# Kernel optimization log

Measured on AMD Instinct MI355X. Metric: run time of the kernel, lower is better.

The kernel has to match this reference:

```python
import jax, jax.numpy as jnp
import numpy as np

VOCAB, EMB, HID, LAT = 32000, 512, 1024, 64
B, S = 64, 512

def setup_inputs() -> dict:
    key = jax.random.key(0)
    ks = jax.random.split(key, 10)
    s_e = 1.0 / np.sqrt(HID)
    s_l = 1.0 / np.sqrt(HID)
    return {
        'input_ids': jax.random.randint(ks[0], (B, S), 0, VOCAB),
        'emb_weight': jax.random.normal(ks[1], (VOCAB, EMB), jnp.float32),
        'w_ih': jax.random.uniform(ks[2], (3 * HID, EMB), jnp.float32, -s_e, s_e),
        'w_hh': jax.random.uniform(ks[3], (3 * HID, HID), jnp.float32, -s_e, s_e),
        'b_ih': jax.random.uniform(ks[4], (3 * HID,), jnp.float32, -s_e, s_e),
        'b_hh': jax.random.uniform(ks[5], (3 * HID,), jnp.float32, -s_e, s_e),
        'w_mean': jax.random.uniform(ks[6], (LAT, HID), jnp.float32, -s_l, s_l),
        'b_mean': jax.random.uniform(ks[7], (LAT,), jnp.float32, -s_l, s_l),
        'w_logv': jax.random.uniform(ks[8], (LAT, HID), jnp.float32, -s_l, s_l),
        'b_logv': jax.random.uniform(ks[9], (LAT,), jnp.float32, -s_l, s_l),
    }

def _gru_mean_hidden(ids, emb_weight, w_ih, w_hh, b_ih, b_hh):
    x = emb_weight[ids]                      # [B, S, E]
    # precompute input-side gate preactivations for all timesteps
    gx = jnp.einsum('bse,ge->bsg', x, w_ih) + b_ih   # [B, S, 3H]
    gx_t = jnp.swapaxes(gx, 0, 1)            # [S, B, 3H] for scan

    def step(h, gx_i):
        gh = h @ w_hh.T + b_hh               # [B, 3H]
        # torch GRU gate order: r, z, n
        r = jax.nn.sigmoid(gx_i[:, :HID] + gh[:, :HID])
        z = jax.nn.sigmoid(gx_i[:, HID:2 * HID] + gh[:, HID:2 * HID])
        n = jnp.tanh(gx_i[:, 2 * HID:] + r * gh[:, 2 * HID:])
        h_new = (1.0 - z) * n + z * h
        return h_new, h_new

    h0 = jnp.zeros((ids.shape[0], HID), gx.dtype)
    _, hs = jax.lax.scan(step, h0, gx_t)      # hs: [S, B, H]
    return jnp.mean(hs, axis=0)               # mean pooling over time -> [B, H]

def reference(input_ids, emb_weight, w_ih, w_hh, b_ih, b_hh, w_mean, b_mean, w_logv, b_logv):
    h = _gru_mean_hidden(input_ids, emb_weight, w_ih, w_hh, b_ih, b_hh)
    mean = h @ w_mean.T + b_mean
    logv = h @ w_logv.T + b_logv
    return (mean, logv)
```

## Files before the change

kernel.cpp:

```cpp
#include <hip/hip_runtime.h>
#include <hip/hip_bf16.h>
#include <stdint.h>
#include <stddef.h>

#define HID   1024
#define NB    64
#define SEQ   512
#define G3    3072
#define EMB   512
#define LAT   64

typedef __attribute__((ext_vector_type(4))) float f32x4;
typedef __attribute__((ext_vector_type(8))) short bfrag;
typedef unsigned long long ull;

__device__ __forceinline__ unsigned short f2bf(float x) {
  union { float f; unsigned u; } v; v.f = x;
  unsigned u = v.u + 0x7fffu + ((v.u >> 16) & 1u);
  return (unsigned short)(u >> 16);
}
__device__ __forceinline__ float bf2f(short s) {
  union { unsigned u; float f; } v; v.u = ((unsigned)(unsigned short)s) << 16;
  return v.f;
}
__device__ __forceinline__ float fsig(float x) {
  return 1.0f / (1.0f + __builtin_exp2f(-1.4426950408889634f * x));
}
__device__ __forceinline__ float ftanh(float x) {
  return 1.0f - 2.0f / (1.0f + __builtin_exp2f(2.8853900817779268f * x));
}
__device__ __forceinline__ void gload_lds16(const void* g, void* l) {
  __builtin_amdgcn_global_load_lds(
      (const __attribute__((address_space(1))) unsigned int*)g,
      (__attribute__((address_space(3))) unsigned int*)l, 16, 0, 0);
}

__global__ void cvt_wih_kernel(const float* __restrict__ in, short* __restrict__ out) {
  int i = (blockIdx.x * 256 + threadIdx.x) * 8;
  f32x4 a = *(const f32x4*)(in + i);
  f32x4 b = *(const f32x4*)(in + i + 4);
  bfrag o;
  o[0]=(short)f2bf(a[0]); o[1]=(short)f2bf(a[1]); o[2]=(short)f2bf(a[2]); o[3]=(short)f2bf(a[3]);
  o[4]=(short)f2bf(b[0]); o[5]=(short)f2bf(b[1]); o[6]=(short)f2bf(b[2]); o[7]=(short)f2bf(b[3]);
  *(bfrag*)(out + i) = o;
}

__global__ void __launch_bounds__(256) gemm_gx_kernel(
    const int* __restrict__ ids, const float* __restrict__ emb,
    const short* __restrict__ wih, short* __restrict__ gx)
{
  const int nt = blockIdx.x, mt = blockIdx.y;
  const int tid = threadIdx.x;
  const int lane = tid & 63, wave = tid >> 6;
  const int wr = wave >> 1, wc = wave & 1;

  __shared__ __align__(16) short A_lds[128 * 48];
  __shared__ __align__(16) short B_lds[128 * 32];
  __shared__ int ids_s[128];

  if (tid < 128) ids_s[tid] = ids[mt * 128 + tid];
  __syncthreads();

  f32x4 acc[4][4];
  #pragma unroll
  for (int i = 0; i < 4; ++i)
    #pragma unroll
    for (int j = 0; j < 4; ++j) acc[i][j] = (f32x4){0.f, 0.f, 0.f, 0.f};

  const int r_stage = tid >> 1;
  const int kh = (tid & 1) * 16;

  #pragma unroll 1
  for (int kc = 0; kc < 16; ++kc) {
    __syncthreads();
    {
      const float* src = emb + (size_t)ids_s[r_stage] * 512 + kc * 32 + kh;
      f32x4 v0 = *(const f32x4*)(src);
      f32x4 v1 = *(const f32x4*)(src + 4);
      f32x4 v2 = *(const f32x4*)(src + 8);
      f32x4 v3 = *(const f32x4*)(src + 12);
      bfrag p0, p1;
      p0[0]=(short)f2bf(v0[0]); p0[1]=(short)f2bf(v0[1]); p0[2]=(short)f2bf(v0[2]); p0[3]=(short)f2bf(v0[3]);
      p0[4]=(short)f2bf(v1[0]); p0[5]=(short)f2bf(v1[1]); p0[6]=(short)f2bf(v1[2]); p0[7]=(short)f2bf(v1[3]);
      p1[0]=(short)f2bf(v2[0]); p1[1]=(short)f2bf(v2[1]); p1[2]=(short)f2bf(v2[2]); p1[3]=(short)f2bf(v2[3]);
      p1[4]=(short)f2bf(v3[0]); p1[5]=(short)f2bf(v3[1]); p1[6]=(short)f2bf(v3[2]); p1[7]=(short)f2bf(v3[3]);
      *(bfrag*)&A_lds[r_stage * 48 + kh]     = p0;
      *(bfrag*)&A_lds[r_stage * 48 + kh + 8] = p1;
    }
    {
      #pragma unroll
      for (int ii = 0; ii < 2; ++ii) {
        int i = wave * 2 + ii;
        const short* src = wih + (size_t)(nt * 128 + i * 16 + (lane >> 2)) * 512
                               + kc * 32 + (lane & 3) * 8;
        gload_lds16((const void*)src, (void*)&B_lds[i * 512]);
      }
    }
    asm volatile("s_waitcnt vmcnt(0)" ::: "memory");
    __syncthreads();

    bfrag a[4], b[4];
    #pragma unroll
    for (int mi = 0; mi < 4; ++mi)
      a[mi] = *(const bfrag*)&A_lds[(wr * 64 + mi * 16 + (lane & 15)) * 48 + (lane >> 4) * 8];
    #pragma unroll
    for (int ni = 0; ni < 4; ++ni)
      b[ni] = *(const bfrag*)&B_lds[(wc * 64 + ni * 16 + (lane & 15)) * 32 + (lane >> 4) * 8];
    #pragma unroll
    for (int mi = 0; mi < 4; ++mi)
      #pragma unroll
      for (int ni = 0; ni < 4; ++ni)
        acc[mi][ni] = __builtin_amdgcn_mfma_f32_16x16x32_bf16(a[mi], b[ni], acc[mi][ni], 0, 0, 0);
  }

  #pragma unroll
  for (int mi = 0; mi < 4; ++mi)
    #pragma unroll
    for (int ni = 0; ni < 4; ++ni)
      #pragma unroll
      for (int r = 0; r < 4; ++r) {
        int m = mt * 128 + wr * 64 + mi * 16 + (lane >> 4) * 4 + r;
        int n = nt * 128 + wc * 64 + ni * 16 + (lane & 15);
        gx[(size_t)m * G3 + n] = (short)f2bf(acc[mi][ni][r]);
      }
}

__global__ void __launch_bounds__(256, 1) gru_scan_kernel(
    const short* __restrict__ gx, const float* __restrict__ whh,
    const float* __restrict__ bihp, const float* __restrict__ bhhp,
    ull* __restrict__ hbuf_q, unsigned int* __restrict__ flags,
    float* __restrict__ hsum)
{
  const int wg   = blockIdx.x;
  const int team = wg >> 6;
  const int cg   = wg & 63;
  const int tid  = threadIdx.x;
  const int lane = tid & 63, wave = tid >> 6;
  const int bl   = lane & 15;
  const int bsub = (lane >> 4) * 4;
  const int jcol = cg * 16 + bl;
  const int bteam = team * 16;

  __shared__ __align__(16) short h_lds[16 * 1024];
  __shared__ __align__(16) float part[3 * 3 * 256];
  __shared__ __align__(16) short hstg[256];

  bfrag wfrag[3][8];
  #pragma unroll
  for (int g = 0; g < 3; ++g) {
    const float* wrow = whh + (size_t)(g * 1024 + jcol) * 1024 + wave * 256 + (lane >> 4) * 8;
    #pragma unroll
    for (int ks = 0; ks < 8; ++ks) {
      const float* p = wrow + ks * 32;
      f32x4 lo = *(const f32x4*)p;
      f32x4 hi = *(const f32x4*)(p + 4);
      bfrag f;
      f[0]=(short)f2bf(lo[0]); f[1]=(short)f2bf(lo[1]); f[2]=(short)f2bf(lo[2]); f[3]=(short)f2bf(lo[3]);
      f[4]=(short)f2bf(hi[0]); f[5]=(short)f2bf(hi[1]); f[6]=(short)f2bf(hi[2]); f[7]=(short)f2bf(hi[3]);
      wfrag[g][ks] = f;
    }
  }
  float bih_r[3], bhh_r[3];
  #pragma unroll
  for (int g = 0; g < 3; ++g) {
    bih_r[g] = bihp[g * 1024 + jcol];
    bhh_r[g] = bhhp[g * 1024 + jcol];
  }

  float hprev[4] = {0.f, 0.f, 0.f, 0.f};
  float hacc[4]  = {0.f, 0.f, 0.f, 0.f};
  const int xorm = (bl & 7) << 4;
  const char* lbase = (const char*)h_lds + bl * 2048;
  unsigned int* fteam = flags + team * 1024;
  unsigned int* myflag = fteam + cg * 16;

  short gxr_[4][3];
  if (wave == 0) {
    #pragma unroll
    for (int r = 0; r < 4; ++r) {
      size_t base = ((size_t)(bteam + bsub + r) * SEQ + 0) * G3 + jcol;
      gxr_[r][0] = gx[base];
      gxr_[r][1] = gx[base + 1024];
      gxr_[r][2] = gx[base + 2048];
    }
  }

  #pragma unroll 1
  for (int s = 0; s < SEQ; ++s) {
    const ull* hsrc = hbuf_q + ((s & 1) ? 16384 : 0) + team * 4096;
    ull*       hdst = hbuf_q + (((s + 1) & 1) ? 16384 : 0) + team * 4096;

    {
      ull hv[16];
      #pragma unroll
      for (int j = 0; j < 16; ++j)
        hv[j] = __hip_atomic_load(hsrc + j * 256 + tid, __ATOMIC_RELAXED,
                                  __HIP_MEMORY_SCOPE_AGENT);
      #pragma unroll
      for (int j = 0; j < 16; ++j) {
        int q  = j * 256 + tid;
        int cgq = q >> 6, b = (q >> 2) & 15, cq = q & 3;
        *(ull*)((char*)h_lds + b * 2048 + ((cgq * 32 + cq * 8) ^ ((b & 7) << 4))) = hv[j];
      }
    }
    __syncthreads();

    f32x4 a0 = {0.f,0.f,0.f,0.f}, a1 = {0.f,0.f,0.f,0.f}, a2 = {0.f,0.f,0.f,0.f};
    #pragma unroll
    for (int ks = 0; ks < 8; ++ks) {
      int k2 = wave * 512 + ks * 64 + (lane >> 4) * 16;
      bfrag af = *(const bfrag*)(lbase + (k2 ^ xorm));
      a0 = __builtin_amdgcn_mfma_f32_16x16x32_bf16(af, wfrag[0][ks], a0, 0, 0, 0);
      a1 = __builtin_amdgcn_mfma_f32_16x16x32_bf16(af, wfrag[1][ks], a1, 0, 0, 0);
      a2 = __builtin_amdgcn_mfma_f32_16x16x32_bf16(af, wfrag[2][ks], a2, 0, 0, 0);
    }
    if (wave) {
      int w1 = wave - 1;
      *(f32x4*)&part[((0 * 3 + w1) * 64 + lane) * 4] = a0;
      *(f32x4*)&part[((1 * 3 + w1) * 64 + lane) * 4] = a1;
      *(f32x4*)&part[((2 * 3 + w1) * 64 + lane) * 4] = a2;
    }
    __syncthreads();

    if (wave == 0) {
      f32x4 s0 = a0, s1 = a1, s2 = a2;
      #pragma unroll
      for (int w1 = 0; w1 < 3; ++w1) {
        s0 += *(const f32x4*)&part[((0 * 3 + w1) * 64 + lane) * 4];
        s1 += *(const f32x4*)&part[((1 * 3 + w1) * 64 + lane) * 4];
        s2 += *(const f32x4*)&part[((2 * 3 + w1) * 64 + lane) * 4];
      }
      #pragma unroll
      for (int r = 0; r < 4; ++r) {
        float ghr = s0[r] + bhh_r[0];
        float ghz = s1[r] + bhh_r[1];
        float ghn = s2[r] + bhh_r[2];
        float rg = fsig(bf2f(gxr_[r][0]) + bih_r[0] + ghr);
        float zg = fsig(bf2f(gxr_[r][1]) + bih_r[1] + ghz);
        float ng = ftanh(bf2f(gxr_[r][2]) + bih_r[2] + rg * ghn);
        float hn = (1.f - zg) * ng + zg * hprev[r];
        hprev[r] = hn;
        hacc[r] += hn;
        hstg[(bsub + r) * 16 + bl] = (short)f2bf(hn);
      }
    }
    __syncthreads();

    if (wave == 1) {
      ull v = ((const ull*)hstg)[lane];
      __hip_atomic_store(hdst + cg * 64 + lane, v, __ATOMIC_RELAXED,
                         __HIP_MEMORY_SCOPE_AGENT);
      asm volatile("s_waitcnt vmcnt(0)" ::: "memory");
      if (lane == 0)
        __hip_atomic_store(myflag, (unsigned)(s + 1), __ATOMIC_RELAXED,
                           __HIP_MEMORY_SCOPE_AGENT);
    }
    if (wave == 0) {
      int sn = (s + 1 < SEQ) ? (s + 1) : s;
      #pragma unroll
      for (int r = 0; r < 4; ++r) {
        size_t base = ((size_t)(bteam + bsub + r) * SEQ + sn) * G3 + jcol;
        gxr_[r][0] = gx[base];
        gxr_[r][1] = gx[base + 1024];
        gxr_[r][2] = gx[base + 2048];
      }
      unsigned tgt = (unsigned)(s + 1);
      for (;;) {
        unsigned v = __hip_atomic_load(fteam + lane * 16, __ATOMIC_RELAXED,
                                       __HIP_MEMORY_SCOPE_AGENT);
        if (__all((int)(v >= tgt))) break;
      }
    }
    __syncthreads();
  }

  if (wave == 0) {
    #pragma unroll
    for (int r = 0; r < 4; ++r)
      hsum[(size_t)(bteam + bsub + r) * 1024 + jcol] = hacc[r] * (1.0f / 512.0f);
  }
}

__global__ void proj_kernel(const float* __restrict__ hbar,
                            const float* __restrict__ wm, const float* __restrict__ bm,
                            const float* __restrict__ wl, const float* __restrict__ bl,
                            float* __restrict__ out)
{
  int b = blockIdx.x, t = threadIdx.x;
  __shared__ float hrow[1024];
  for (int k = t; k < 1024; k += 128) hrow[k] = hbar[(size_t)b * 1024 + k];
  __syncthreads();
  int j = t & 63;
  const float* w = (t < 64) ? (wm + (size_t)j * 1024) : (wl + (size_t)j * 1024);
  float acc = (t < 64) ? bm[j] : bl[j];
  for (int k = 0; k < 1024; k += 4) {
    f32x4 wv = *(const f32x4*)(w + k);
    acc += hrow[k] * wv[0] + hrow[k+1] * wv[1] + hrow[k+2] * wv[2] + hrow[k+3] * wv[3];
  }
  out[(size_t)((t < 64) ? 0 : 4096) + b * 64 + j] = acc;
}

extern "C" void kernel_launch(void* const* d_in, const int* in_sizes, int n_in,
                              void* d_out, int out_size, void* d_ws, size_t ws_size,
                              hipStream_t stream) {
  const int*   ids   = (const int*)d_in[0];
  const float* emb   = (const float*)d_in[1];
  const float* w_ih  = (const float*)d_in[2];
  const float* w_hh  = (const float*)d_in[3];
  const float* b_ih  = (const float*)d_in[4];
  const float* b_hh  = (const float*)d_in[5];
  const float* w_mean= (const float*)d_in[6];
  const float* b_mean= (const float*)d_in[7];
  const float* w_logv= (const float*)d_in[8];
  const float* b_logv= (const float*)d_in[9];
  float* out = (float*)d_out;

  char* ws = (char*)d_ws;
  unsigned int* flags = (unsigned int*)(ws);
  ull* hbuf_q        = (ull*)(ws + 16384);
  float* hsum        = (float*)(ws + 16384 + 262144);
  short* wihb        = (short*)(ws + 16384 + 262144 + 262144);
  short* gxbuf       = (short*)(ws + 16384 + 262144 + 262144 + 3145728);

  hipMemsetAsync(ws, 0, 16384 + 262144, stream);

  cvt_wih_kernel<<<768, 256, 0, stream>>>(w_ih, wihb);
  gemm_gx_kernel<<<dim3(24, 256), 256, 0, stream>>>(ids, emb, wihb, gxbuf);
  gru_scan_kernel<<<256, 256, 0, stream>>>(gxbuf, w_hh, b_ih, b_hh, hbuf_q, flags, hsum);
  proj_kernel<<<64, 128, 0, stream>>>(hsum, w_mean, b_mean, w_logv, b_logv, out);
}
```

Before: 2.031 ms.

## Replace flag-based grid barrier with epoch-tagged hidden-state words

Each published bf16 hidden value is now packed with a 16-bit step epoch in its upper half, so consumers spin directly on the data words until the expected epoch appears. This removes the separate per-workgroup flag store, the vmcnt wait before it, the flag polling loop and two block-wide barriers per timestep. The cost is doubled hidden-state traffic, since each value now occupies 32 bits, plus per-word polling. The design relies on relaxed 64-bit atomics not tearing and on the epoch not wrapping within 512 steps.

```diff
diff --git a/kernel.cpp b/kernel.cpp
--- a/kernel.cpp
+++ b/kernel.cpp
@@ -128,8 +128,7 @@
 __global__ void __launch_bounds__(256, 1) gru_scan_kernel(
     const short* __restrict__ gx, const float* __restrict__ whh,
     const float* __restrict__ bihp, const float* __restrict__ bhhp,
-    ull* __restrict__ hbuf_q, unsigned int* __restrict__ flags,
-    float* __restrict__ hsum)
+    ull* __restrict__ hbuf_q, float* __restrict__ hsum)
 {
   const int wg   = blockIdx.x;
   const int team = wg >> 6;
@@ -143,7 +142,7 @@
 
   __shared__ __align__(16) short h_lds[16 * 1024];
   __shared__ __align__(16) float part[3 * 3 * 256];
-  __shared__ __align__(16) short hstg[256];
+  __shared__ __align__(16) unsigned hstg[256];
 
   bfrag wfrag[3][8];
   #pragma unroll
@@ -171,8 +170,6 @@
   float hacc[4]  = {0.f, 0.f, 0.f, 0.f};
   const int xorm = (bl & 7) << 4;
   const char* lbase = (const char*)h_lds + bl * 2048;
-  unsigned int* fteam = flags + team * 1024;
-  unsigned int* myflag = fteam + cg * 16;
 
   short gxr_[4][3];
   if (wave == 0) {
@@ -187,23 +184,34 @@
 
   #pragma unroll 1
   for (int s = 0; s < SEQ; ++s) {
-    const ull* hsrc = hbuf_q + ((s & 1) ? 16384 : 0) + team * 4096;
-    ull*       hdst = hbuf_q + (((s + 1) & 1) ? 16384 : 0) + team * 4096;
+    const ull* qsrc = hbuf_q + ((s & 1) ? 32768 : 0) + team * 8192;
+    ull*       qdst = hbuf_q + (((s + 1) & 1) ? 32768 : 0) + team * 8192;
 
     {
-      ull hv[16];
-      #pragma unroll
-      for (int j = 0; j < 16; ++j)
-        hv[j] = __hip_atomic_load(hsrc + j * 256 + tid, __ATOMIC_RELAXED,
-                                  __HIP_MEMORY_SCOPE_AGENT);
-      #pragma unroll
-      for (int j = 0; j < 16; ++j) {
-        int q  = j * 256 + tid;
-        int cgq = q >> 6, b = (q >> 2) & 15, cq = q & 3;
-        *(ull*)((char*)h_lds + b * 2048 + ((cgq * 32 + cq * 8) ^ ((b & 7) << 4))) = hv[j];
-      }
-    }
-    __syncthreads();
+      const ull want = (ull)(unsigned)s * 0x0001000000010000ull;
+      ull hv[32];
+      #pragma unroll
+      for (int b = 0; b < 16; ++b) {
+        hv[2*b]   = __hip_atomic_load(qsrc + b * 512 + wave * 128 + lane,
+                                      __ATOMIC_RELAXED, __HIP_MEMORY_SCOPE_AGENT);
+        hv[2*b+1] = __hip_atomic_load(qsrc + b * 512 + wave * 128 + 64 + lane,
+                                      __ATOMIC_RELAXED, __HIP_MEMORY_SCOPE_AGENT);
+      }
+      #pragma unroll
+      for (int b = 0; b < 16; ++b) {
+        #pragma unroll
+        for (int t = 0; t < 2; ++t) {
+          ull q = hv[2*b+t];
+          while ((q & 0xFFFF0000FFFF0000ull) != want)
+            q = __hip_atomic_load(qsrc + b * 512 + wave * 128 + t * 64 + lane,
+                                  __ATOMIC_RELAXED, __HIP_MEMORY_SCOPE_AGENT);
+          unsigned lo = (unsigned)q, hi = (unsigned)(q >> 32);
+          unsigned w2 = (lo & 0xFFFFu) | (hi << 16);
+          int kb = wave * 512 + t * 256 + lane * 4;
+          *(unsigned*)((char*)h_lds + b * 2048 + (kb ^ ((b & 7) << 4))) = w2;
+        }
+      }
+    }
 
     f32x4 a0 = {0.f,0.f,0.f,0.f}, a1 = {0.f,0.f,0.f,0.f}, a2 = {0.f,0.f,0.f,0.f};
     #pragma unroll
@@ -230,6 +238,7 @@
         s1 += *(const f32x4*)&part[((1 * 3 + w1) * 64 + lane) * 4];
         s2 += *(const f32x4*)&part[((2 * 3 + w1) * 64 + lane) * 4];
       }
+      unsigned ep = ((unsigned)(s + 1)) << 16;
       #pragma unroll
       for (int r = 0; r < 4; ++r) {
         float ghr = s0[r] + bhh_r[0];
@@ -241,19 +250,18 @@
         float hn = (1.f - zg) * ng + zg * hprev[r];
         hprev[r] = hn;
         hacc[r] += hn;
-        hstg[(bsub + r) * 16 + bl] = (short)f2bf(hn);
+        hstg[(bsub + r) * 16 + bl] = ep | (unsigned)f2bf(hn);
       }
     }
     __syncthreads();
 
     if (wave == 1) {
-      ull v = ((const ull*)hstg)[lane];
-      __hip_atomic_store(hdst + cg * 64 + lane, v, __ATOMIC_RELAXED,
-                         __HIP_MEMORY_SCOPE_AGENT);
-      asm volatile("s_waitcnt vmcnt(0)" ::: "memory");
-      if (lane == 0)
-        __hip_atomic_store(myflag, (unsigned)(s + 1), __ATOMIC_RELAXED,
-                           __HIP_MEMORY_SCOPE_AGENT);
+      int b = lane >> 2, c4 = lane & 3;
+      const ull* src = (const ull*)hstg + b * 8 + c4 * 2;
+      ull v0 = src[0], v1 = src[1];
+      ull* dst = qdst + b * 512 + cg * 8 + c4 * 2;
+      __hip_atomic_store(dst,     v0, __ATOMIC_RELAXED, __HIP_MEMORY_SCOPE_AGENT);
+      __hip_atomic_store(dst + 1, v1, __ATOMIC_RELAXED, __HIP_MEMORY_SCOPE_AGENT);
     }
     if (wave == 0) {
       int sn = (s + 1 < SEQ) ? (s + 1) : s;
@@ -264,14 +272,7 @@
         gxr_[r][1] = gx[base + 1024];
         gxr_[r][2] = gx[base + 2048];
       }
-      unsigned tgt = (unsigned)(s + 1);
-      for (;;) {
-        unsigned v = __hip_atomic_load(fteam + lane * 16, __ATOMIC_RELAXED,
-                                       __HIP_MEMORY_SCOPE_AGENT);
-        if (__all((int)(v >= tgt))) break;
-      }
-    }
-    __syncthreads();
+    }
   }
 
   if (wave == 0) {
@@ -316,16 +317,15 @@
   float* out = (float*)d_out;
 
   char* ws = (char*)d_ws;
-  unsigned int* flags = (unsigned int*)(ws);
-  ull* hbuf_q        = (ull*)(ws + 16384);
-  float* hsum        = (float*)(ws + 16384 + 262144);
-  short* wihb        = (short*)(ws + 16384 + 262144 + 262144);
-  short* gxbuf       = (short*)(ws + 16384 + 262144 + 262144 + 3145728);
-
-  hipMemsetAsync(ws, 0, 16384 + 262144, stream);
+  ull*   hbuf_q = (ull*)(ws);
+  float* hsum   = (float*)(ws + 524288);
+  short* wihb   = (short*)(ws + 524288 + 262144);
+  short* gxbuf  = (short*)(ws + 524288 + 262144 + 3145728);
+
+  hipMemsetAsync(ws, 0, 524288, stream);
 
   cvt_wih_kernel<<<768, 256, 0, stream>>>(w_ih, wihb);
   gemm_gx_kernel<<<dim3(24, 256), 256, 0, stream>>>(ids, emb, wihb, gxbuf);
-  gru_scan_kernel<<<256, 256, 0, stream>>>(gxbuf, w_hh, b_ih, b_hh, hbuf_q, flags, hsum);
+  gru_scan_kernel<<<256, 256, 0, stream>>>(gxbuf, w_hh, b_ih, b_hh, hbuf_q, hsum);
   proj_kernel<<<64, 128, 0, stream>>>(hsum, w_mean, b_mean, w_logv, b_logv, out);
 }
```

After: 5.960 ms. 2.93x slower.

## Use a two-level grid barrier and drop the block barrier after loading h

Applied to the files above, without the earlier changes.

The cross-workgroup step barrier becomes two-level. Workgroup 0 of each team polls all 64 per-workgroup flags and then publishes a single team-level 'super' flag, which the other workgroups poll instead of scanning all 64 flags. This cuts atomic polling traffic on the shared flag lines. In exchange it adds one extra serial hop of global-memory latency to every timestep barrier. Separately, the hidden-state load is remapped so each wave writes exactly the LDS slice it later reads for its MFMA k-range, which lets the __syncthreads between the LDS fill and the MFMAs be removed.

```diff
diff --git a/kernel.cpp b/kernel.cpp
--- a/kernel.cpp
+++ b/kernel.cpp
@@ -129,7 +129,7 @@
     const short* __restrict__ gx, const float* __restrict__ whh,
     const float* __restrict__ bihp, const float* __restrict__ bhhp,
     ull* __restrict__ hbuf_q, unsigned int* __restrict__ flags,
-    float* __restrict__ hsum)
+    unsigned int* __restrict__ superf, float* __restrict__ hsum)
 {
   const int wg   = blockIdx.x;
   const int team = wg >> 6;
@@ -171,8 +171,15 @@
   float hacc[4]  = {0.f, 0.f, 0.f, 0.f};
   const int xorm = (bl & 7) << 4;
   const char* lbase = (const char*)h_lds + bl * 2048;
-  unsigned int* fteam = flags + team * 1024;
+  unsigned int* fteam  = flags + team * 1024;
   unsigned int* myflag = fteam + cg * 16;
+  unsigned int* mysuper = superf + team * 16;
+  const bool is_agg = (cg == 0);
+
+  const int st_b  = lane >> 2;
+  const int st_c4 = lane & 3;
+  char* const st_base = (char*)h_lds + st_b * 2048;
+  const int st_swz = (st_b & 7) << 4;
 
   short gxr_[4][3];
   if (wave == 0) {
@@ -194,16 +201,14 @@
       ull hv[16];
       #pragma unroll
       for (int j = 0; j < 16; ++j)
-        hv[j] = __hip_atomic_load(hsrc + j * 256 + tid, __ATOMIC_RELAXED,
-                                  __HIP_MEMORY_SCOPE_AGENT);
+        hv[j] = __hip_atomic_load(hsrc + wave * 1024 + j * 64 + lane,
+                                  __ATOMIC_RELAXED, __HIP_MEMORY_SCOPE_AGENT);
       #pragma unroll
       for (int j = 0; j < 16; ++j) {
-        int q  = j * 256 + tid;
-        int cgq = q >> 6, b = (q >> 2) & 15, cq = q & 3;
-        *(ull*)((char*)h_lds + b * 2048 + ((cgq * 32 + cq * 8) ^ ((b & 7) << 4))) = hv[j];
-      }
-    }
-    __syncthreads();
+        int cgq = wave * 16 + j;
+        *(ull*)(st_base + (((cgq * 32 + st_c4 * 8)) ^ st_swz)) = hv[j];
+      }
+    }
 
     f32x4 a0 = {0.f,0.f,0.f,0.f}, a1 = {0.f,0.f,0.f,0.f}, a2 = {0.f,0.f,0.f,0.f};
     #pragma unroll
@@ -265,10 +270,18 @@
         gxr_[r][2] = gx[base + 2048];
       }
       unsigned tgt = (unsigned)(s + 1);
-      for (;;) {
-        unsigned v = __hip_atomic_load(fteam + lane * 16, __ATOMIC_RELAXED,
-                                       __HIP_MEMORY_SCOPE_AGENT);
-        if (__all((int)(v >= tgt))) break;
+      if (is_agg) {
+        for (;;) {
+          unsigned v = __hip_atomic_load(fteam + lane * 16, __ATOMIC_RELAXED,
+                                         __HIP_MEMORY_SCOPE_AGENT);
+          if (__all((int)(v >= tgt))) break;
+        }
+        if (lane == 0)
+          __hip_atomic_store(mysuper, tgt, __ATOMIC_RELAXED,
+                             __HIP_MEMORY_SCOPE_AGENT);
+      } else {
+        while (__hip_atomic_load(mysuper, __ATOMIC_RELAXED,
+                                 __HIP_MEMORY_SCOPE_AGENT) < tgt) { }
       }
     }
     __syncthreads();
@@ -316,16 +329,18 @@
   float* out = (float*)d_out;
 
   char* ws = (char*)d_ws;
-  unsigned int* flags = (unsigned int*)(ws);
-  ull* hbuf_q        = (ull*)(ws + 16384);
-  float* hsum        = (float*)(ws + 16384 + 262144);
-  short* wihb        = (short*)(ws + 16384 + 262144 + 262144);
-  short* gxbuf       = (short*)(ws + 16384 + 262144 + 262144 + 3145728);
-
-  hipMemsetAsync(ws, 0, 16384 + 262144, stream);
+  unsigned int* superf = (unsigned int*)(ws);
+  unsigned int* flags  = (unsigned int*)(ws + 1024);
+  ull* hbuf_q        = (ull*)(ws + 1024 + 16384);
+  float* hsum        = (float*)(ws + 1024 + 16384 + 262144);
+  short* wihb        = (short*)(ws + 1024 + 16384 + 262144 + 262144);
+  short* gxbuf       = (short*)(ws + 1024 + 16384 + 262144 + 262144 + 3145728);
+
+  hipMemsetAsync(ws, 0, 1024 + 16384 + 262144, stream);
 
   cvt_wih_kernel<<<768, 256, 0, stream>>>(w_ih, wihb);
   gemm_gx_kernel<<<dim3(24, 256), 256, 0, stream>>>(ids, emb, wihb, gxbuf);
-  gru_scan_kernel<<<256, 256, 0, stream>>>(gxbuf, w_hh, b_ih, b_hh, hbuf_q, flags, hsum);
+  gru_scan_kernel<<<256, 256, 0, stream>>>(gxbuf, w_hh, b_ih, b_hh,
+                                           hbuf_q, flags, superf, hsum);
   proj_kernel<<<64, 128, 0, stream>>>(hsum, w_mean, b_mean, w_logv, b_logv, out);
 }
```

New measurement: 2.149 ms. 5.8% more time.

## Merge GRU scan workgroups: 32 columns per 512-thread block, halving grid and flags

Applied to the files above, without the earlier changes.

Restructures the persistent GRU scan so each workgroup handles 32 hidden columns with 8 waves (two column halves times four K-quarters) instead of 16 columns with 4 waves. The grid shrinks from 256 to 128 blocks, and each team now synchronises through 32 flags instead of 64. This halves the per-step flag polling and the redundant loads of h into LDS across the chip. In exchange each block holds twice the weight registers across more waves, and the grid now occupies only half as many CUs.

```diff
diff --git a/kernel.cpp b/kernel.cpp
--- a/kernel.cpp
+++ b/kernel.cpp
@@ -125,30 +125,31 @@
       }
 }
 
-__global__ void __launch_bounds__(256, 1) gru_scan_kernel(
+__global__ void __launch_bounds__(512, 1) gru_scan_kernel(
     const short* __restrict__ gx, const float* __restrict__ whh,
     const float* __restrict__ bihp, const float* __restrict__ bhhp,
     ull* __restrict__ hbuf_q, unsigned int* __restrict__ flags,
     float* __restrict__ hsum)
 {
-  const int wg   = blockIdx.x;
-  const int team = wg >> 6;
-  const int cg   = wg & 63;
+  const int team = blockIdx.x >> 5;
+  const int cg2  = blockIdx.x & 31;
   const int tid  = threadIdx.x;
-  const int lane = tid & 63, wave = tid >> 6;
+  const int lane = tid & 63, wv = tid >> 6;
+  const int ch   = wv >> 2;
+  const int kq   = wv & 3;
   const int bl   = lane & 15;
   const int bsub = (lane >> 4) * 4;
-  const int jcol = cg * 16 + bl;
+  const int jcol = cg2 * 32 + ch * 16 + bl;
   const int bteam = team * 16;
 
   __shared__ __align__(16) short h_lds[16 * 1024];
-  __shared__ __align__(16) float part[3 * 3 * 256];
-  __shared__ __align__(16) short hstg[256];
+  __shared__ __align__(16) float part[2 * 3 * 3 * 256];
+  __shared__ __align__(16) short hstg[16 * 32];
 
   bfrag wfrag[3][8];
   #pragma unroll
   for (int g = 0; g < 3; ++g) {
-    const float* wrow = whh + (size_t)(g * 1024 + jcol) * 1024 + wave * 256 + (lane >> 4) * 8;
+    const float* wrow = whh + (size_t)(g * 1024 + jcol) * 1024 + kq * 256 + (lane >> 4) * 8;
     #pragma unroll
     for (int ks = 0; ks < 8; ++ks) {
       const float* p = wrow + ks * 32;
@@ -171,11 +172,11 @@
   float hacc[4]  = {0.f, 0.f, 0.f, 0.f};
   const int xorm = (bl & 7) << 4;
   const char* lbase = (const char*)h_lds + bl * 2048;
-  unsigned int* fteam = flags + team * 1024;
-  unsigned int* myflag = fteam + cg * 16;
+  unsigned int* fteam  = flags + team * 512;
+  unsigned int* myflag = fteam + cg2 * 16;
 
   short gxr_[4][3];
-  if (wave == 0) {
+  if (kq == 0) {
     #pragma unroll
     for (int r = 0; r < 4; ++r) {
       size_t base = ((size_t)(bteam + bsub + r) * SEQ + 0) * G3 + jcol;
@@ -191,14 +192,14 @@
     ull*       hdst = hbuf_q + (((s + 1) & 1) ? 16384 : 0) + team * 4096;
 
     {
-      ull hv[16];
-      #pragma unroll
-      for (int j = 0; j < 16; ++j)
-        hv[j] = __hip_atomic_load(hsrc + j * 256 + tid, __ATOMIC_RELAXED,
+      ull hv[8];
+      #pragma unroll
+      for (int j = 0; j < 8; ++j)
+        hv[j] = __hip_atomic_load(hsrc + j * 512 + tid, __ATOMIC_RELAXED,
                                   __HIP_MEMORY_SCOPE_AGENT);
       #pragma unroll
-      for (int j = 0; j < 16; ++j) {
-        int q  = j * 256 + tid;
+      for (int j = 0; j < 8; ++j) {
+        int q  = j * 512 + tid;
         int cgq = q >> 6, b = (q >> 2) & 15, cq = q & 3;
         *(ull*)((char*)h_lds + b * 2048 + ((cgq * 32 + cq * 8) ^ ((b & 7) << 4))) = hv[j];
       }
@@ -208,27 +209,27 @@
     f32x4 a0 = {0.f,0.f,0.f,0.f}, a1 = {0.f,0.f,0.f,0.f}, a2 = {0.f,0.f,0.f,0.f};
     #pragma unroll
     for (int ks = 0; ks < 8; ++ks) {
-      int k2 = wave * 512 + ks * 64 + (lane >> 4) * 16;
+      int k2 = kq * 512 + ks * 64 + (lane >> 4) * 16;
       bfrag af = *(const bfrag*)(lbase + (k2 ^ xorm));
       a0 = __builtin_amdgcn_mfma_f32_16x16x32_bf16(af, wfrag[0][ks], a0, 0, 0, 0);
       a1 = __builtin_amdgcn_mfma_f32_16x16x32_bf16(af, wfrag[1][ks], a1, 0, 0, 0);
       a2 = __builtin_amdgcn_mfma_f32_16x16x32_bf16(af, wfrag[2][ks], a2, 0, 0, 0);
     }
-    if (wave) {
-      int w1 = wave - 1;
-      *(f32x4*)&part[((0 * 3 + w1) * 64 + lane) * 4] = a0;
-      *(f32x4*)&part[((1 * 3 + w1) * 64 + lane) * 4] = a1;
-      *(f32x4*)&part[((2 * 3 + w1) * 64 + lane) * 4] = a2;
-    }
-    __syncthreads();
-
-    if (wave == 0) {
+    if (kq) {
+      int w1 = kq - 1;
+      *(f32x4*)&part[((ch * 9 + 0 * 3 + w1) * 64 + lane) * 4] = a0;
+      *(f32x4*)&part[((ch * 9 + 1 * 3 + w1) * 64 + lane) * 4] = a1;
+      *(f32x4*)&part[((ch * 9 + 2 * 3 + w1) * 64 + lane) * 4] = a2;
+    }
+    __syncthreads();
+
+    if (kq == 0) {
       f32x4 s0 = a0, s1 = a1, s2 = a2;
       #pragma unroll
       for (int w1 = 0; w1 < 3; ++w1) {
-        s0 += *(const f32x4*)&part[((0 * 3 + w1) * 64 + lane) * 4];
-        s1 += *(const f32x4*)&part[((1 * 3 + w1) * 64 + lane) * 4];
-        s2 += *(const f32x4*)&part[((2 * 3 + w1) * 64 + lane) * 4];
+        s0 += *(const f32x4*)&part[((ch * 9 + 0 * 3 + w1) * 64 + lane) * 4];
+        s1 += *(const f32x4*)&part[((ch * 9 + 1 * 3 + w1) * 64 + lane) * 4];
+        s2 += *(const f32x4*)&part[((ch * 9 + 2 * 3 + w1) * 64 + lane) * 4];
       }
       #pragma unroll
       for (int r = 0; r < 4; ++r) {
@@ -241,21 +242,25 @@
         float hn = (1.f - zg) * ng + zg * hprev[r];
         hprev[r] = hn;
         hacc[r] += hn;
-        hstg[(bsub + r) * 16 + bl] = (short)f2bf(hn);
-      }
-    }
-    __syncthreads();
-
-    if (wave == 1) {
-      ull v = ((const ull*)hstg)[lane];
-      __hip_atomic_store(hdst + cg * 64 + lane, v, __ATOMIC_RELAXED,
+        hstg[(bsub + r) * 32 + ch * 16 + bl] = (short)f2bf(hn);
+      }
+    }
+    __syncthreads();
+
+    if (wv == 1) {
+      const ull* hq = (const ull*)hstg;
+      ull v0 = hq[(lane >> 2) * 8 + (lane & 3)];
+      ull v1 = hq[(lane >> 2) * 8 + 4 + (lane & 3)];
+      __hip_atomic_store(hdst + cg2 * 128 + lane,      v0, __ATOMIC_RELAXED,
+                         __HIP_MEMORY_SCOPE_AGENT);
+      __hip_atomic_store(hdst + cg2 * 128 + 64 + lane, v1, __ATOMIC_RELAXED,
                          __HIP_MEMORY_SCOPE_AGENT);
       asm volatile("s_waitcnt vmcnt(0)" ::: "memory");
       if (lane == 0)
         __hip_atomic_store(myflag, (unsigned)(s + 1), __ATOMIC_RELAXED,
                            __HIP_MEMORY_SCOPE_AGENT);
     }
-    if (wave == 0) {
+    if (kq == 0) {
       int sn = (s + 1 < SEQ) ? (s + 1) : s;
       #pragma unroll
       for (int r = 0; r < 4; ++r) {
@@ -264,9 +269,11 @@
         gxr_[r][1] = gx[base + 1024];
         gxr_[r][2] = gx[base + 2048];
       }
+    }
+    if (wv == 0) {
       unsigned tgt = (unsigned)(s + 1);
       for (;;) {
-        unsigned v = __hip_atomic_load(fteam + lane * 16, __ATOMIC_RELAXED,
+        unsigned v = __hip_atomic_load(fteam + (lane & 31) * 16, __ATOMIC_RELAXED,
                                        __HIP_MEMORY_SCOPE_AGENT);
         if (__all((int)(v >= tgt))) break;
       }
@@ -274,7 +281,7 @@
     __syncthreads();
   }
 
-  if (wave == 0) {
+  if (kq == 0) {
     #pragma unroll
     for (int r = 0; r < 4; ++r)
       hsum[(size_t)(bteam + bsub + r) * 1024 + jcol] = hacc[r] * (1.0f / 512.0f);
@@ -317,15 +324,15 @@
 
   char* ws = (char*)d_ws;
   unsigned int* flags = (unsigned int*)(ws);
-  ull* hbuf_q        = (ull*)(ws + 16384);
-  float* hsum        = (float*)(ws + 16384 + 262144);
-  short* wihb        = (short*)(ws + 16384 + 262144 + 262144);
-  short* gxbuf       = (short*)(ws + 16384 + 262144 + 262144 + 3145728);
-
-  hipMemsetAsync(ws, 0, 16384 + 262144, stream);
+  ull* hbuf_q        = (ull*)(ws + 8192);
+  float* hsum        = (float*)(ws + 8192 + 262144);
+  short* wihb        = (short*)(ws + 8192 + 262144 + 262144);
+  short* gxbuf       = (short*)(ws + 8192 + 262144 + 262144 + 3145728);
+
+  hipMemsetAsync(ws, 0, 8192 + 262144, stream);
 
   cvt_wih_kernel<<<768, 256, 0, stream>>>(w_ih, wihb);
   gemm_gx_kernel<<<dim3(24, 256), 256, 0, stream>>>(ids, emb, wihb, gxbuf);
-  gru_scan_kernel<<<256, 256, 0, stream>>>(gxbuf, w_hh, b_ih, b_hh, hbuf_q, flags, hsum);
+  gru_scan_kernel<<<128, 512, 0, stream>>>(gxbuf, w_hh, b_ih, b_hh, hbuf_q, flags, hsum);
   proj_kernel<<<64, 128, 0, stream>>>(hsum, w_mean, b_mean, w_logv, b_logv, out);
 }
```

New measurement: 2.336 ms. 1.15x slower.
